# Kernel tuning notes

Hardware: AMD Instinct MI355X
Metric: run time of the kernel (lower is better)

Reference implementation:

```python
import jax, jax.numpy as jnp
import numpy as np


def reference(x, edge_index, edge_attr, W, b):
    """PyG GCNConv: out = D^{-1/2} (A + I) D^{-1/2} X W + b.

    x: [N, Din] node features
    edge_index: [2, E] int (row=source, col=target)
    edge_attr: [E] edge weights
    W: [Din, Dout], b: [Dout]
    """
    N = x.shape[0]
    # add self-loops with weight 1 (PyG fill_value=1.0)
    loop = jnp.arange(N, dtype=edge_index.dtype)
    row = jnp.concatenate([edge_index[0], loop])
    col = jnp.concatenate([edge_index[1], loop])
    w = jnp.concatenate([edge_attr, jnp.ones((N,), dtype=edge_attr.dtype)])

    # symmetric normalization: norm_e = d[row]^-1/2 * w_e * d[col]^-1/2
    deg = jax.ops.segment_sum(w, col, num_segments=N)
    dis = jnp.where(deg > 0, jax.lax.rsqrt(jnp.where(deg > 0, deg, 1.0)), 0.0)
    norm = dis[row] * w * dis[col]

    # linear projection first (Din == Dout, cheaper either way), then
    # gather-scale-scatter aggregation at targets
    h = x @ W                                   # [N, Dout]
    msg = h[row] * norm[:, None]                # [E+N, Dout]
    out = jax.ops.segment_sum(msg, col, num_segments=N)  # [N, Dout]
    return out + b


def setup_inputs() -> dict:
    key = jax.random.key(0)
    k1, k2, k3, k4 = jax.random.split(key, 4)
    N, E, Din, Dout = 100000, 1600000, 128, 128
    x = jax.random.normal(k1, (N, Din), dtype=jnp.float32)
    edge_index = jax.random.randint(k2, (2, E), 0, N, dtype=jnp.int64)
    edge_attr = jax.random.uniform(k3, (E,), dtype=jnp.float32)
    # Glorot init like PyG Linear default
    W = jax.random.normal(k4, (Din, Dout), dtype=jnp.float32) * (1.0 / np.sqrt(Din))
    b = jnp.zeros((Dout,), dtype=jnp.float32)
    return {"x": x, "edge_index": edge_index, "edge_attr": edge_attr, "W": W, "b": b}
```

## Files before the change

### kernel.cpp

```cpp
#include <hip/hip_runtime.h>


#define ELEMS_PER_SCAN_BLOCK 2048
#define CHUNK 4096

typedef __attribute__((ext_vector_type(8))) short short8;
typedef __attribute__((ext_vector_type(4))) float f32x4;

__device__ inline unsigned short f2bf(float f) {
    unsigned u = __float_as_uint(f);
    u += 0x7fffu + ((u >> 16) & 1u);
    return (unsigned short)(u >> 16);
}
__device__ inline float bf_lo(unsigned u) { return __uint_as_float(u << 16); }
__device__ inline float bf_hi(unsigned u) { return __uint_as_float(u & 0xffff0000u); }

__global__ __launch_bounds__(256) void k_hist(const int* __restrict__ col,
                                              int* __restrict__ histg,
                                              int E, int NC, int NBLK) {
    __shared__ int lh[1024];
    int t = threadIdx.x, blk = blockIdx.x;
    for (int i = t; i < 1024; i += 256) lh[i] = 0;
    __syncthreads();
    int base = blk * CHUNK;
    #pragma unroll
    for (int i = 0; i < CHUNK / 256; ++i) {
        int e = base + i * 256 + t;
        if (e < E) atomicAdd(&lh[col[e] >> 7], 1);
    }
    __syncthreads();
    for (int b = t; b < NC; b += 256) histg[b * NBLK + blk] = lh[b];
}

__device__ inline int wave_incl_scan(int x, int lane) {
    #pragma unroll
    for (int d = 1; d < 64; d <<= 1) {
        int y = __shfl_up(x, d, 64);
        if (lane >= d) x += y;
    }
    return x;
}

__global__ void k_scan1(const int* __restrict__ in, int* __restrict__ out,
                        int* __restrict__ bsum, int M) {
    __shared__ int wsum[4];
    __shared__ int woff[4];
    int t = threadIdx.x, lane = t & 63, wid = t >> 6;
    int base = blockIdx.x * ELEMS_PER_SCAN_BLOCK + t * 8;
    int v[8];
    #pragma unroll
    for (int i = 0; i < 8; ++i) v[i] = (base + i < M) ? in[base + i] : 0;
    int run = 0;
    #pragma unroll
    for (int i = 0; i < 8; ++i) { int x = v[i]; v[i] = run; run += x; }
    int incl = wave_incl_scan(run, lane);
    int excl = incl - run;
    if (lane == 63) wsum[wid] = incl;
    __syncthreads();
    if (t == 0) {
        int r = 0;
        #pragma unroll
        for (int w = 0; w < 4; ++w) { int s = wsum[w]; woff[w] = r; r += s; }
        bsum[blockIdx.x] = r;
    }
    __syncthreads();
    int off = woff[wid] + excl;
    #pragma unroll
    for (int i = 0; i < 8; ++i)
        if (base + i < M) out[base + i] = v[i] + off;
}

__global__ void k_scan2(const int* __restrict__ bsum, int* __restrict__ boff, int NB) {
    __shared__ int wsum[4];
    __shared__ int woff[4];
    int t = threadIdx.x, lane = t & 63, wid = t >> 6;
    int x = (t < NB) ? bsum[t] : 0;
    int incl = wave_incl_scan(x, lane);
    int excl = incl - x;
    if (lane == 63) wsum[wid] = incl;
    __syncthreads();
    if (t == 0) {
        int r = 0;
        #pragma unroll
        for (int w = 0; w < 4; ++w) { int s = wsum[w]; woff[w] = r; r += s; }
    }
    __syncthreads();
    if (t < NB) boff[t] = woff[wid] + excl;
}

__global__ void k_scan3(int* __restrict__ arr, const int* __restrict__ boff, int M) {
    int t = threadIdx.x;
    int base = blockIdx.x * ELEMS_PER_SCAN_BLOCK + t * 8;
    int off = boff[blockIdx.x];
    #pragma unroll
    for (int i = 0; i < 8; ++i) {
        int idx = base + i;
        if (idx < M) arr[idx] += off;
    }
}

__global__ __launch_bounds__(256) void k_place(const int* __restrict__ row,
                                               const int* __restrict__ col,
                                               const float* __restrict__ wgt,
                                               const int* __restrict__ histg,
                                               int2* __restrict__ srw,
                                               int E, int NC, int NBLK) {
    __shared__ int lo[1024];
    int t = threadIdx.x, blk = blockIdx.x;
    for (int b = t; b < NC; b += 256) lo[b] = histg[b * NBLK + blk];
    __syncthreads();
    int base = blk * CHUNK;
    #pragma unroll
    for (int i = 0; i < CHUNK / 256; ++i) {
        int e = base + i * 256 + t;
        if (e < E) {
            int c = col[e];
            int pos = atomicAdd(&lo[c >> 7], 1);
            srw[pos] = make_int2(((c & 127) << 17) | row[e], __float_as_int(wgt[e]));
        }
    }
}

__global__ __launch_bounds__(256) void k_fine(const int* __restrict__ histg,
                                              const int2* __restrict__ srw,
                                              int* __restrict__ rowptr,
                                              float* __restrict__ dis,
                                              int2* __restrict__ spack,
                                              int E, int N, int NC, int NBLK) {
    __shared__ int cnt128[128];
    __shared__ float degf[128];
    __shared__ int cur128[128];
    __shared__ int wtot[2];
    int t = threadIdx.x, b = blockIdx.x;
    int nb = b << 7;
    int start = histg[b * NBLK];
    int end = (b == NC - 1) ? E : histg[(b + 1) * NBLK];
    if (t < 128) { cnt128[t] = 0; degf[t] = 1.0f; }
    __syncthreads();
    for (int j = start + t; j < end; j += 256) {
        int2 s = srw[j];
        int c = s.x >> 17;
        atomicAdd(&cnt128[c], 1);
        atomicAdd(&degf[c], __int_as_float(s.y));
    }
    __syncthreads();
    int v = 0, incl = 0;
    if (t < 128) {
        v = cnt128[t];
        incl = wave_incl_scan(v, t & 63);
        if ((t & 63) == 63) wtot[t >> 6] = incl;
    }
    __syncthreads();
    if (t < 128) {
        int excl = incl - v + ((t >= 64) ? wtot[0] : 0);
        int p = start + excl;
        cur128[t] = p;
        int n = nb + t;
        if (n < N) {
            rowptr[n] = p;
            dis[n] = rsqrtf(degf[t]);
        }
    }
    if (t == 0 && b == NC - 1) rowptr[N] = E;
    __syncthreads();
    for (int j = start + t; j < end; j += 256) {
        int2 s = srw[j];
        int c = s.x >> 17;
        int pos = atomicAdd(&cur128[c], 1);
        spack[pos] = make_int2(s.x & 0x1FFFF, s.y);
    }
}

__global__ void k_wprep(const float* __restrict__ W, unsigned short* __restrict__ Wtg) {
    int n = blockIdx.x;
    int k = threadIdx.x;
    Wtg[n * 128 + k] = f2bf(W[k * 128 + n]);
}

__global__ __launch_bounds__(256) void k_gemm(const float* __restrict__ x,
                                              const unsigned short* __restrict__ Wtg,
                                              unsigned short* __restrict__ h, int N) {
    __shared__ short Xs[64][136];
    __shared__ short Ws[128][136];
    int t = threadIdx.x;
    int lane = t & 63, wid = t >> 6;
    int row0 = blockIdx.x * 64;
    {
        int r = t >> 2;
        int kseg = (t & 3) * 32;
        int gr = row0 + r;
        const float4* src = (const float4*)(x + (size_t)gr * 128 + kseg);
        #pragma unroll
        for (int i = 0; i < 4; ++i) {
            float4 v0 = make_float4(0.f, 0.f, 0.f, 0.f), v1 = v0;
            if (gr < N) { v0 = src[2 * i]; v1 = src[2 * i + 1]; }
            short8 p;
            p[0] = (short)f2bf(v0.x); p[1] = (short)f2bf(v0.y);
            p[2] = (short)f2bf(v0.z); p[3] = (short)f2bf(v0.w);
            p[4] = (short)f2bf(v1.x); p[5] = (short)f2bf(v1.y);
            p[6] = (short)f2bf(v1.z); p[7] = (short)f2bf(v1.w);
            *(short8*)&Xs[r][kseg + 8 * i] = p;
        }
    }
    {
        int n = t >> 1;
        int seg = (t & 1) * 64;
        const short* wsrc = (const short*)Wtg + n * 128 + seg;
        #pragma unroll
        for (int i = 0; i < 8; ++i)
            *(short8*)&Ws[n][seg + 8 * i] = *(const short8*)(wsrc + 8 * i);
    }
    __syncthreads();

    int q = lane >> 4;
    int m = lane & 15;
    f32x4 acc[8];
    #pragma unroll
    for (int tde = 0; tde < 8; ++tde) acc[tde] = (f32x4){0.f, 0.f, 0.f, 0.f};
    #pragma unroll
    for (int kc = 0; kc < 128; kc += 32) {
        short8 af = *(const short8*)&Xs[wid * 16 + m][kc + q * 8];
        #pragma unroll
        for (int tde = 0; tde < 8; ++tde) {
            short8 bf = *(const short8*)&Ws[tde * 16 + m][kc + q * 8];
            acc[tde] = __builtin_amdgcn_mfma_f32_16x16x32_bf16(af, bf, acc[tde], 0, 0, 0);
        }
    }
    #pragma unroll
    for (int r = 0; r < 4; ++r) {
        int grow = row0 + wid * 16 + q * 4 + r;
        if (grow < N) {
            #pragma unroll
            for (int tde = 0; tde < 8; ++tde)
                h[(size_t)grow * 128 + tde * 16 + m] = f2bf(acc[tde][r]);
        }
    }
}

__global__ __launch_bounds__(256) void k_gather(const unsigned int* __restrict__ hb,
                                                const float* __restrict__ dis,
                                                const int* __restrict__ rowptr,
                                                const long* __restrict__ spackl,
                                                const float* __restrict__ bias,
                                                float* __restrict__ out, int N) {
    int gid = blockIdx.x * blockDim.x + threadIdx.x;
    int node = gid >> 6;
    int lane = gid & 63;
    if (node >= N) return;
    node = __builtin_amdgcn_readfirstlane(node);

    float dn = dis[node];
    unsigned u = hb[(size_t)node * 64 + lane];
    float2 acc;
    acc.x = dn * bf_lo(u);
    acc.y = dn * bf_hi(u);

    int jb = rowptr[node], je = rowptr[node + 1];
    int j = jb;
    for (; j + 8 <= je; j += 8) {
        long q0 = __builtin_nontemporal_load(spackl + j);
        long q1 = __builtin_nontemporal_load(spackl + j + 1);
        long q2 = __builtin_nontemporal_load(spackl + j + 2);
        long q3 = __builtin_nontemporal_load(spackl + j + 3);
        long q4 = __builtin_nontemporal_load(spackl + j + 4);
        long q5 = __builtin_nontemporal_load(spackl + j + 5);
        long q6 = __builtin_nontemporal_load(spackl + j + 6);
        long q7 = __builtin_nontemporal_load(spackl + j + 7);
        int r0 = __builtin_amdgcn_readfirstlane((int)q0);
        int r1 = __builtin_amdgcn_readfirstlane((int)q1);
        int r2 = __builtin_amdgcn_readfirstlane((int)q2);
        int r3 = __builtin_amdgcn_readfirstlane((int)q3);
        int r4 = __builtin_amdgcn_readfirstlane((int)q4);
        int r5 = __builtin_amdgcn_readfirstlane((int)q5);
        int r6 = __builtin_amdgcn_readfirstlane((int)q6);
        int r7 = __builtin_amdgcn_readfirstlane((int)q7);
        unsigned u0 = hb[(size_t)r0 * 64 + lane];
        unsigned u1 = hb[(size_t)r1 * 64 + lane];
        unsigned u2 = hb[(size_t)r2 * 64 + lane];
        unsigned u3 = hb[(size_t)r3 * 64 + lane];
        unsigned u4 = hb[(size_t)r4 * 64 + lane];
        unsigned u5 = hb[(size_t)r5 * 64 + lane];
        unsigned u6 = hb[(size_t)r6 * 64 + lane];
        unsigned u7 = hb[(size_t)r7 * 64 + lane];
        float a0 = dis[r0] * __uint_as_float((unsigned)(q0 >> 32));
        float a1 = dis[r1] * __uint_as_float((unsigned)(q1 >> 32));
        float a2 = dis[r2] * __uint_as_float((unsigned)(q2 >> 32));
        float a3 = dis[r3] * __uint_as_float((unsigned)(q3 >> 32));
        float a4 = dis[r4] * __uint_as_float((unsigned)(q4 >> 32));
        float a5 = dis[r5] * __uint_as_float((unsigned)(q5 >> 32));
        float a6 = dis[r6] * __uint_as_float((unsigned)(q6 >> 32));
        float a7 = dis[r7] * __uint_as_float((unsigned)(q7 >> 32));
        acc.x = fmaf(a0, bf_lo(u0), acc.x); acc.y = fmaf(a0, bf_hi(u0), acc.y);
        acc.x = fmaf(a1, bf_lo(u1), acc.x); acc.y = fmaf(a1, bf_hi(u1), acc.y);
        acc.x = fmaf(a2, bf_lo(u2), acc.x); acc.y = fmaf(a2, bf_hi(u2), acc.y);
        acc.x = fmaf(a3, bf_lo(u3), acc.x); acc.y = fmaf(a3, bf_hi(u3), acc.y);
        acc.x = fmaf(a4, bf_lo(u4), acc.x); acc.y = fmaf(a4, bf_hi(u4), acc.y);
        acc.x = fmaf(a5, bf_lo(u5), acc.x); acc.y = fmaf(a5, bf_hi(u5), acc.y);
        acc.x = fmaf(a6, bf_lo(u6), acc.x); acc.y = fmaf(a6, bf_hi(u6), acc.y);
        acc.x = fmaf(a7, bf_lo(u7), acc.x); acc.y = fmaf(a7, bf_hi(u7), acc.y);
    }
    for (; j < je; ++j) {
        long q = __builtin_nontemporal_load(spackl + j);
        int r = __builtin_amdgcn_readfirstlane((int)q);
        unsigned uu = hb[(size_t)r * 64 + lane];
        float a = dis[r] * __uint_as_float((unsigned)(q >> 32));
        acc.x = fmaf(a, bf_lo(uu), acc.x);
        acc.y = fmaf(a, bf_hi(uu), acc.y);
    }

    int c0 = lane * 2;
    float2 bv = *(const float2*)(bias + c0);
    float2 o;
    o.x = bv.x + dn * acc.x;
    o.y = bv.y + dn * acc.y;
    union { float2 f; double d; } cvt;
    cvt.f = o;
    __builtin_nontemporal_store(cvt.d, (double*)(out + (size_t)node * 128 + c0));
}

extern "C" void kernel_launch(void* const* d_in, const int* in_sizes, int n_in,
                              void* d_out, int out_size, void* d_ws, size_t ws_size,
                              hipStream_t stream) {
    const float* x     = (const float*)d_in[0];
    const int*   eidx  = (const int*)d_in[1];
    const float* eattr = (const float*)d_in[2];
    const float* W     = (const float*)d_in[3];
    const float* bias  = (const float*)d_in[4];
    int N = in_sizes[0] / 128;
    int E = in_sizes[2];
    const int* row = eidx;
    const int* col = eidx + E;

    int NC = (N + 127) >> 7;
    int NBLK = (E + CHUNK - 1) / CHUNK;

    char* p = (char*)d_ws;
    auto carve = [&](size_t bytes) {
        char* q = p;
        p += (bytes + 255) & ~(size_t)255;
        return q;
    };
    unsigned short* h   = (unsigned short*)carve((size_t)N * 128 * sizeof(unsigned short));
    unsigned short* Wtg = (unsigned short*)carve(128 * 128 * sizeof(unsigned short));
    float* dis    = (float*)carve((size_t)N * sizeof(float));
    int*   rowptr = (int*)carve((size_t)(N + 1) * sizeof(int));
    int*   histg  = (int*)carve((size_t)NC * NBLK * sizeof(int));
    int2*  srw    = (int2*)carve((size_t)E * sizeof(int2));
    int2*  spack  = (int2*)carve((size_t)E * sizeof(int2));
    int*   bsum   = (int*)carve(256 * sizeof(int));
    int*   boff   = (int*)carve(256 * sizeof(int));

    int M = NC * NBLK;
    int NBs = (M + ELEMS_PER_SCAN_BLOCK - 1) / ELEMS_PER_SCAN_BLOCK;

    k_hist<<<NBLK, 256, 0, stream>>>(col, histg, E, NC, NBLK);
    k_scan1<<<NBs, 256, 0, stream>>>(histg, histg, bsum, M);
    k_scan2<<<1, 256, 0, stream>>>(bsum, boff, NBs);
    k_scan3<<<NBs, 256, 0, stream>>>(histg, boff, M);
    k_place<<<NBLK, 256, 0, stream>>>(row, col, eattr, histg, srw, E, NC, NBLK);
    k_fine<<<NC, 256, 0, stream>>>(histg, srw, rowptr, dis, spack, E, N, NC, NBLK);
    k_wprep<<<128, 128, 0, stream>>>(W, Wtg);
    k_gemm<<<(N + 63) / 64, 256, 0, stream>>>(x, Wtg, h, N);
    {
        size_t threads = (size_t)N * 64;
        int blocks = (int)((threads + 255) / 256);
        k_gather<<<blocks, 256, 0, stream>>>((const unsigned int*)h, dis, rowptr,
                                             (const long*)spack, bias, (float*)d_out, N);
    }
}
```

Before: 274.0 us.

## Slice bf16 h into column panels and gather edges in parallel per wave

The GEMM now writes h as eight column-panel slices of 16 bf16 features each, so one slice of all nodes (about 3.2 MB) is much smaller than the full matrix. Block IDs interleave the slice index so concurrent blocks work on the same slice, which is meant to keep the random gathers L2-resident. Each wave takes one node and one slice: the 64 lanes split into 8 edge slots of 8 lanes, process 16 edges per iteration and combine results with xor shuffles. In exchange, h is read eight times, and every edge record plus dis value is loaded eight times, once per slice. The row index is masked to 17 bits, which assumes N stays below 131072.

```diff
diff --git a/kernel.cpp b/kernel.cpp
--- a/kernel.cpp
+++ b/kernel.cpp
@@ -232,90 +232,70 @@
         if (grow < N) {
             #pragma unroll
             for (int tde = 0; tde < 8; ++tde)
-                h[(size_t)grow * 128 + tde * 16 + m] = f2bf(acc[tde][r]);
-        }
-    }
-}
-
-__global__ __launch_bounds__(256) void k_gather(const unsigned int* __restrict__ hb,
+                h[((size_t)tde * N + grow) * 16 + m] = f2bf(acc[tde][r]);
+        }
+    }
+}
+
+__global__ __launch_bounds__(256) void k_gather(const unsigned int* __restrict__ hs,
                                                 const float* __restrict__ dis,
                                                 const int* __restrict__ rowptr,
                                                 const long* __restrict__ spackl,
                                                 const float* __restrict__ bias,
                                                 float* __restrict__ out, int N) {
-    int gid = blockIdx.x * blockDim.x + threadIdx.x;
-    int node = gid >> 6;
-    int lane = gid & 63;
+    int t = threadIdx.x;
+    int lane = t & 63, wid = t >> 6;
+    int s = blockIdx.x & 7;
+    int node = (blockIdx.x >> 3) * 4 + wid;
     if (node >= N) return;
-    node = __builtin_amdgcn_readfirstlane(node);
+    int slot = lane >> 3;
+    int cp = lane & 7;
+    const unsigned int* hsl = hs + (size_t)s * N * 8;
 
     float dn = dis[node];
-    unsigned u = hb[(size_t)node * 64 + lane];
-    float2 acc;
-    acc.x = dn * bf_lo(u);
-    acc.y = dn * bf_hi(u);
-
     int jb = rowptr[node], je = rowptr[node + 1];
-    int j = jb;
-    for (; j + 8 <= je; j += 8) {
-        long q0 = __builtin_nontemporal_load(spackl + j);
-        long q1 = __builtin_nontemporal_load(spackl + j + 1);
-        long q2 = __builtin_nontemporal_load(spackl + j + 2);
-        long q3 = __builtin_nontemporal_load(spackl + j + 3);
-        long q4 = __builtin_nontemporal_load(spackl + j + 4);
-        long q5 = __builtin_nontemporal_load(spackl + j + 5);
-        long q6 = __builtin_nontemporal_load(spackl + j + 6);
-        long q7 = __builtin_nontemporal_load(spackl + j + 7);
-        int r0 = __builtin_amdgcn_readfirstlane((int)q0);
-        int r1 = __builtin_amdgcn_readfirstlane((int)q1);
-        int r2 = __builtin_amdgcn_readfirstlane((int)q2);
-        int r3 = __builtin_amdgcn_readfirstlane((int)q3);
-        int r4 = __builtin_amdgcn_readfirstlane((int)q4);
-        int r5 = __builtin_amdgcn_readfirstlane((int)q5);
-        int r6 = __builtin_amdgcn_readfirstlane((int)q6);
-        int r7 = __builtin_amdgcn_readfirstlane((int)q7);
-        unsigned u0 = hb[(size_t)r0 * 64 + lane];
-        unsigned u1 = hb[(size_t)r1 * 64 + lane];
-        unsigned u2 = hb[(size_t)r2 * 64 + lane];
-        unsigned u3 = hb[(size_t)r3 * 64 + lane];
-        unsigned u4 = hb[(size_t)r4 * 64 + lane];
-        unsigned u5 = hb[(size_t)r5 * 64 + lane];
-        unsigned u6 = hb[(size_t)r6 * 64 + lane];
-        unsigned u7 = hb[(size_t)r7 * 64 + lane];
-        float a0 = dis[r0] * __uint_as_float((unsigned)(q0 >> 32));
-        float a1 = dis[r1] * __uint_as_float((unsigned)(q1 >> 32));
-        float a2 = dis[r2] * __uint_as_float((unsigned)(q2 >> 32));
-        float a3 = dis[r3] * __uint_as_float((unsigned)(q3 >> 32));
-        float a4 = dis[r4] * __uint_as_float((unsigned)(q4 >> 32));
-        float a5 = dis[r5] * __uint_as_float((unsigned)(q5 >> 32));
-        float a6 = dis[r6] * __uint_as_float((unsigned)(q6 >> 32));
-        float a7 = dis[r7] * __uint_as_float((unsigned)(q7 >> 32));
-        acc.x = fmaf(a0, bf_lo(u0), acc.x); acc.y = fmaf(a0, bf_hi(u0), acc.y);
-        acc.x = fmaf(a1, bf_lo(u1), acc.x); acc.y = fmaf(a1, bf_hi(u1), acc.y);
-        acc.x = fmaf(a2, bf_lo(u2), acc.x); acc.y = fmaf(a2, bf_hi(u2), acc.y);
-        acc.x = fmaf(a3, bf_lo(u3), acc.x); acc.y = fmaf(a3, bf_hi(u3), acc.y);
-        acc.x = fmaf(a4, bf_lo(u4), acc.x); acc.y = fmaf(a4, bf_hi(u4), acc.y);
-        acc.x = fmaf(a5, bf_lo(u5), acc.x); acc.y = fmaf(a5, bf_hi(u5), acc.y);
-        acc.x = fmaf(a6, bf_lo(u6), acc.x); acc.y = fmaf(a6, bf_hi(u6), acc.y);
-        acc.x = fmaf(a7, bf_lo(u7), acc.x); acc.y = fmaf(a7, bf_hi(u7), acc.y);
-    }
-    for (; j < je; ++j) {
-        long q = __builtin_nontemporal_load(spackl + j);
-        int r = __builtin_amdgcn_readfirstlane((int)q);
-        unsigned uu = hb[(size_t)r * 64 + lane];
-        float a = dis[r] * __uint_as_float((unsigned)(q >> 32));
-        acc.x = fmaf(a, bf_lo(uu), acc.x);
-        acc.y = fmaf(a, bf_hi(uu), acc.y);
-    }
-
-    int c0 = lane * 2;
-    float2 bv = *(const float2*)(bias + c0);
-    float2 o;
-    o.x = bv.x + dn * acc.x;
-    o.y = bv.y + dn * acc.y;
-    union { float2 f; double d; } cvt;
-    cvt.f = o;
-    __builtin_nontemporal_store(cvt.d, (double*)(out + (size_t)node * 128 + c0));
+    float2 acc = make_float2(0.f, 0.f);
+
+    for (int j0 = jb; j0 < je; j0 += 16) {
+        int e0 = j0 + slot;
+        int e1 = e0 + 8;
+        int c0 = (e0 < je) ? e0 : je - 1;
+        int c1 = (e1 < je) ? e1 : je - 1;
+        long q0 = spackl[c0];
+        long q1 = spackl[c1];
+        int r0 = (int)q0 & 0x1FFFF;
+        int r1 = (int)q1 & 0x1FFFF;
+        float w0 = __uint_as_float((unsigned)((unsigned long)q0 >> 32));
+        float w1 = __uint_as_float((unsigned)((unsigned long)q1 >> 32));
+        float a0 = (e0 < je) ? dis[r0] * w0 : 0.f;
+        float a1 = (e1 < je) ? dis[r1] * w1 : 0.f;
+        unsigned v0 = hsl[(size_t)r0 * 8 + cp];
+        unsigned v1 = hsl[(size_t)r1 * 8 + cp];
+        acc.x = fmaf(a0, bf_lo(v0), acc.x);
+        acc.y = fmaf(a0, bf_hi(v0), acc.y);
+        acc.x = fmaf(a1, bf_lo(v1), acc.x);
+        acc.y = fmaf(a1, bf_hi(v1), acc.y);
+    }
+
+    #pragma unroll
+    for (int d = 8; d < 64; d <<= 1) {
+        acc.x += __shfl_xor(acc.x, d, 64);
+        acc.y += __shfl_xor(acc.y, d, 64);
+    }
+
+    unsigned vs = hsl[(size_t)node * 8 + cp];
+    float tx = acc.x + dn * bf_lo(vs);
+    float ty = acc.y + dn * bf_hi(vs);
+    if (slot == 0) {
+        int col0 = s * 16 + cp * 2;
+        float2 bv = *(const float2*)(bias + col0);
+        float2 o;
+        o.x = bv.x + dn * tx;
+        o.y = bv.y + dn * ty;
+        union { float2 f; double d; } cvt;
+        cvt.f = o;
+        __builtin_nontemporal_store(cvt.d, (double*)(out + (size_t)node * 128 + col0));
+    }
 }
 
 extern "C" void kernel_launch(void* const* d_in, const int* in_sizes, int n_in,
@@ -362,8 +342,7 @@
     k_wprep<<<128, 128, 0, stream>>>(W, Wtg);
     k_gemm<<<(N + 63) / 64, 256, 0, stream>>>(x, Wtg, h, N);
     {
-        size_t threads = (size_t)N * 64;
-        int blocks = (int)((threads + 255) / 256);
+        int blocks = ((N + 3) >> 2) * 8;
         k_gather<<<blocks, 256, 0, stream>>>((const unsigned int*)h, dis, rowptr,
                                              (const long*)spack, bias, (float*)d_out, N);
     }
```

Result: slower. 487.5 us (+77.9%).

## Stage bucketed edges in LDS for coalesced scatter, prefetch edge packs in aggregation

Applied to the files above, without the earlier changes.

The bucket placement kernel now builds a local histogram and prefix scan per chunk and sorts edges into shared memory. It then writes them out contiguously per bucket, replacing scattered global writes with more coalesced ones. The chunk size is halved so the LDS staging buffer fits, and the scan block is doubled to cover the larger histogram. The aggregation loop software-pipelines the next group of packed edge loads ahead of the gather and FMAs. The costs are more LDS use, extra barriers and a second pass over col in k_place.

```diff
diff --git a/kernel.cpp b/kernel.cpp
--- a/kernel.cpp
+++ b/kernel.cpp
@@ -1,8 +1,8 @@
 #include <hip/hip_runtime.h>
 
 
-#define ELEMS_PER_SCAN_BLOCK 2048
-#define CHUNK 4096
+#define ELEMS_PER_SCAN_BLOCK 4096
+#define CHUNK 2048
 
 typedef __attribute__((ext_vector_type(8))) short short8;
 typedef __attribute__((ext_vector_type(4))) float f32x4;
@@ -46,13 +46,13 @@
     __shared__ int wsum[4];
     __shared__ int woff[4];
     int t = threadIdx.x, lane = t & 63, wid = t >> 6;
-    int base = blockIdx.x * ELEMS_PER_SCAN_BLOCK + t * 8;
-    int v[8];
-    #pragma unroll
-    for (int i = 0; i < 8; ++i) v[i] = (base + i < M) ? in[base + i] : 0;
+    int base = blockIdx.x * ELEMS_PER_SCAN_BLOCK + t * 16;
+    int v[16];
+    #pragma unroll
+    for (int i = 0; i < 16; ++i) v[i] = (base + i < M) ? in[base + i] : 0;
     int run = 0;
     #pragma unroll
-    for (int i = 0; i < 8; ++i) { int x = v[i]; v[i] = run; run += x; }
+    for (int i = 0; i < 16; ++i) { int x = v[i]; v[i] = run; run += x; }
     int incl = wave_incl_scan(run, lane);
     int excl = incl - run;
     if (lane == 63) wsum[wid] = incl;
@@ -66,7 +66,7 @@
     __syncthreads();
     int off = woff[wid] + excl;
     #pragma unroll
-    for (int i = 0; i < 8; ++i)
+    for (int i = 0; i < 16; ++i)
         if (base + i < M) out[base + i] = v[i] + off;
 }
 
@@ -90,10 +90,10 @@
 
 __global__ void k_scan3(int* __restrict__ arr, const int* __restrict__ boff, int M) {
     int t = threadIdx.x;
-    int base = blockIdx.x * ELEMS_PER_SCAN_BLOCK + t * 8;
+    int base = blockIdx.x * ELEMS_PER_SCAN_BLOCK + t * 16;
     int off = boff[blockIdx.x];
     #pragma unroll
-    for (int i = 0; i < 8; ++i) {
+    for (int i = 0; i < 16; ++i) {
         int idx = base + i;
         if (idx < M) arr[idx] += off;
     }
@@ -105,19 +105,61 @@
                                                const int* __restrict__ histg,
                                                int2* __restrict__ srw,
                                                int E, int NC, int NBLK) {
-    __shared__ int lo[1024];
+    __shared__ int lcnt[1024];
+    __shared__ int gadj[1024];
+    __shared__ int2 stage[CHUNK];
+    __shared__ int sdst[CHUNK];
+    __shared__ int wsum[4];
+    __shared__ int woff[4];
     int t = threadIdx.x, blk = blockIdx.x;
-    for (int b = t; b < NC; b += 256) lo[b] = histg[b * NBLK + blk];
-    __syncthreads();
+    int lane = t & 63, wid = t >> 6;
     int base = blk * CHUNK;
+    int nE = min(CHUNK, E - base);
+    for (int b = t; b < 1024; b += 256) lcnt[b] = 0;
+    __syncthreads();
+    #pragma unroll
+    for (int i = 0; i < CHUNK / 256; ++i) {
+        int e = base + i * 256 + t;
+        if (e < E) atomicAdd(&lcnt[col[e] >> 7], 1);
+    }
+    __syncthreads();
+    int c4[4];
+    int sum = 0;
+    #pragma unroll
+    for (int i = 0; i < 4; ++i) { int v = lcnt[t * 4 + i]; c4[i] = sum; sum += v; }
+    int incl = wave_incl_scan(sum, lane);
+    int excl = incl - sum;
+    if (lane == 63) wsum[wid] = incl;
+    __syncthreads();
+    if (t == 0) {
+        int r = 0;
+        #pragma unroll
+        for (int w = 0; w < 4; ++w) { int s = wsum[w]; woff[w] = r; r += s; }
+    }
+    __syncthreads();
+    int tb = woff[wid] + excl;
+    #pragma unroll
+    for (int i = 0; i < 4; ++i) {
+        int idx = t * 4 + i;
+        int b0 = tb + c4[i];
+        int gb = (idx < NC) ? histg[idx * NBLK + blk] : 0;
+        gadj[idx] = gb - b0;
+        lcnt[idx] = b0;
+    }
+    __syncthreads();
     #pragma unroll
     for (int i = 0; i < CHUNK / 256; ++i) {
         int e = base + i * 256 + t;
         if (e < E) {
             int c = col[e];
-            int pos = atomicAdd(&lo[c >> 7], 1);
-            srw[pos] = make_int2(((c & 127) << 17) | row[e], __float_as_int(wgt[e]));
+            int slot = atomicAdd(&lcnt[c >> 7], 1);
+            stage[slot] = make_int2(((c & 127) << 17) | row[e], __float_as_int(wgt[e]));
+            sdst[slot] = gadj[c >> 7] + slot;
         }
+    }
+    __syncthreads();
+    for (int s_ = t; s_ < nE; s_ += 256) {
+        srw[sdst[s_]] = stage[s_];
     }
 }
 
@@ -257,15 +299,18 @@
 
     int jb = rowptr[node], je = rowptr[node + 1];
     int j = jb;
+    long q0, q1, q2, q3, q4, q5, q6, q7;
+    if (j + 8 <= je) {
+        q0 = __builtin_nontemporal_load(spackl + j);
+        q1 = __builtin_nontemporal_load(spackl + j + 1);
+        q2 = __builtin_nontemporal_load(spackl + j + 2);
+        q3 = __builtin_nontemporal_load(spackl + j + 3);
+        q4 = __builtin_nontemporal_load(spackl + j + 4);
+        q5 = __builtin_nontemporal_load(spackl + j + 5);
+        q6 = __builtin_nontemporal_load(spackl + j + 6);
+        q7 = __builtin_nontemporal_load(spackl + j + 7);
+    }
     for (; j + 8 <= je; j += 8) {
-        long q0 = __builtin_nontemporal_load(spackl + j);
-        long q1 = __builtin_nontemporal_load(spackl + j + 1);
-        long q2 = __builtin_nontemporal_load(spackl + j + 2);
-        long q3 = __builtin_nontemporal_load(spackl + j + 3);
-        long q4 = __builtin_nontemporal_load(spackl + j + 4);
-        long q5 = __builtin_nontemporal_load(spackl + j + 5);
-        long q6 = __builtin_nontemporal_load(spackl + j + 6);
-        long q7 = __builtin_nontemporal_load(spackl + j + 7);
         int r0 = __builtin_amdgcn_readfirstlane((int)q0);
         int r1 = __builtin_amdgcn_readfirstlane((int)q1);
         int r2 = __builtin_amdgcn_readfirstlane((int)q2);
@@ -282,14 +327,23 @@
         unsigned u5 = hb[(size_t)r5 * 64 + lane];
         unsigned u6 = hb[(size_t)r6 * 64 + lane];
         unsigned u7 = hb[(size_t)r7 * 64 + lane];
-        float a0 = dis[r0] * __uint_as_float((unsigned)(q0 >> 32));
-        float a1 = dis[r1] * __uint_as_float((unsigned)(q1 >> 32));
-        float a2 = dis[r2] * __uint_as_float((unsigned)(q2 >> 32));
-        float a3 = dis[r3] * __uint_as_float((unsigned)(q3 >> 32));
-        float a4 = dis[r4] * __uint_as_float((unsigned)(q4 >> 32));
-        float a5 = dis[r5] * __uint_as_float((unsigned)(q5 >> 32));
-        float a6 = dis[r6] * __uint_as_float((unsigned)(q6 >> 32));
-        float a7 = dis[r7] * __uint_as_float((unsigned)(q7 >> 32));
+        int jn = (j + 16 <= je) ? j + 8 : j;
+        long n0 = __builtin_nontemporal_load(spackl + jn);
+        long n1 = __builtin_nontemporal_load(spackl + jn + 1);
+        long n2 = __builtin_nontemporal_load(spackl + jn + 2);
+        long n3 = __builtin_nontemporal_load(spackl + jn + 3);
+        long n4 = __builtin_nontemporal_load(spackl + jn + 4);
+        long n5 = __builtin_nontemporal_load(spackl + jn + 5);
+        long n6 = __builtin_nontemporal_load(spackl + jn + 6);
+        long n7 = __builtin_nontemporal_load(spackl + jn + 7);
+        float a0 = dis[r0] * __uint_as_float((unsigned)((unsigned long)q0 >> 32));
+        float a1 = dis[r1] * __uint_as_float((unsigned)((unsigned long)q1 >> 32));
+        float a2 = dis[r2] * __uint_as_float((unsigned)((unsigned long)q2 >> 32));
+        float a3 = dis[r3] * __uint_as_float((unsigned)((unsigned long)q3 >> 32));
+        float a4 = dis[r4] * __uint_as_float((unsigned)((unsigned long)q4 >> 32));
+        float a5 = dis[r5] * __uint_as_float((unsigned)((unsigned long)q5 >> 32));
+        float a6 = dis[r6] * __uint_as_float((unsigned)((unsigned long)q6 >> 32));
+        float a7 = dis[r7] * __uint_as_float((unsigned)((unsigned long)q7 >> 32));
         acc.x = fmaf(a0, bf_lo(u0), acc.x); acc.y = fmaf(a0, bf_hi(u0), acc.y);
         acc.x = fmaf(a1, bf_lo(u1), acc.x); acc.y = fmaf(a1, bf_hi(u1), acc.y);
         acc.x = fmaf(a2, bf_lo(u2), acc.x); acc.y = fmaf(a2, bf_hi(u2), acc.y);
@@ -298,12 +352,13 @@
         acc.x = fmaf(a5, bf_lo(u5), acc.x); acc.y = fmaf(a5, bf_hi(u5), acc.y);
         acc.x = fmaf(a6, bf_lo(u6), acc.x); acc.y = fmaf(a6, bf_hi(u6), acc.y);
         acc.x = fmaf(a7, bf_lo(u7), acc.x); acc.y = fmaf(a7, bf_hi(u7), acc.y);
+        q0 = n0; q1 = n1; q2 = n2; q3 = n3; q4 = n4; q5 = n5; q6 = n6; q7 = n7;
     }
     for (; j < je; ++j) {
         long q = __builtin_nontemporal_load(spackl + j);
         int r = __builtin_amdgcn_readfirstlane((int)q);
         unsigned uu = hb[(size_t)r * 64 + lane];
-        float a = dis[r] * __uint_as_float((unsigned)(q >> 32));
+        float a = dis[r] * __uint_as_float((unsigned)((unsigned long)q >> 32));
         acc.x = fmaf(a, bf_lo(uu), acc.x);
         acc.y = fmaf(a, bf_hi(uu), acc.y);
     }
```

Result: no change. 270.2 us (-1.4%).
